# Kernel optimization log

Measured on AMD Instinct MI355X. Metric: run time of the kernel, lower is better.

## Reference

```python
import jax, jax.numpy as jnp
import numpy as np

DIM = 1024
N_HEADS = 16
HEAD_DIM = DIM // N_HEADS  # 64
B, T = 2, 2048


def setup_inputs() -> dict:
    key = jax.random.key(0)
    k1, k2, k3, k4, k5 = jax.random.split(key, 5)
    x = jax.random.normal(k1, (B, T, DIM), dtype=jnp.float32)
    cos = jax.random.uniform(k2, (1, 1, T, HEAD_DIM // 2), dtype=jnp.float32)
    sin = jax.random.uniform(k3, (1, 1, T, HEAD_DIM // 2), dtype=jnp.float32)
    # torch Linear weights: y = x @ W.T ; qkv: [3*dim, dim], out_proj: [dim, dim]
    w_qkv = jax.random.normal(k4, (3 * DIM, DIM), dtype=jnp.float32) * 0.02
    w_out = jax.random.normal(k5, (DIM, DIM), dtype=jnp.float32) * 0.02
    return {"x": x, "cos": cos, "sin": sin, "w_qkv": w_qkv, "w_out": w_out}


def _rope(t, cos, sin):
    # t: [B, H, T, D]; cos/sin broadcast as [1,1,T,D/2]
    t1, t2 = jnp.split(t, 2, axis=-1)
    return jnp.concatenate([t1 * cos - t2 * sin, t1 * sin + t2 * cos], axis=-1)


def reference(x, cos, sin, w_qkv, w_out):
    Bb, Tt, C = x.shape
    qkv = x @ w_qkv.T                                    # [B, T, 3C]
    q, k, v = jnp.split(qkv, 3, axis=-1)
    def heads(t):
        return t.reshape(Bb, Tt, N_HEADS, HEAD_DIM).transpose(0, 2, 1, 3)
    q, k, v = heads(q), heads(k), heads(v)               # [B, H, T, D]
    q = _rope(q, cos, sin)
    k = _rope(k, cos, sin)
    scale = 1.0 / jnp.sqrt(jnp.float32(HEAD_DIM))
    scores = jnp.einsum("bhqd,bhkd->bhqk", q, k) * scale  # [B, H, T, T]
    causal = jnp.tril(jnp.ones((Tt, Tt), dtype=bool))
    scores = jnp.where(causal[None, None], scores, jnp.float32(-jnp.inf))
    attn = jax.nn.softmax(scores, axis=-1)
    out = jnp.einsum("bhqk,bhkd->bhqd", attn, v)          # [B, H, T, D]
    out = out.transpose(0, 2, 1, 3).reshape(Bb, Tt, C)
    return out @ w_out.T
```

## Files before the change

kernel.cpp:

```cpp
#include <hip/hip_runtime.h>

#define DIMC 1024
#define NH   16
#define HD   64
#define BSZ  2
#define TSZ  2048
#define MROWS (BSZ*TSZ)

typedef __attribute__((ext_vector_type(8))) short s16x8;
typedef __attribute__((ext_vector_type(4))) float f32x4;

__device__ __forceinline__ float b2f(unsigned short u) {
  return __uint_as_float(((unsigned)u) << 16);
}
__device__ __forceinline__ unsigned short f2b(float f) {
  unsigned x = __float_as_uint(f);
  unsigned r = x + 0x7fffu + ((x >> 16) & 1u);
  return (unsigned short)(r >> 16);
}
__device__ __forceinline__ unsigned pk2(float a, float b) {
  unsigned r;
  asm("v_cvt_pk_bf16_f32 %0, %1, %2" : "=v"(r) : "v"(a), "v"(b));
  return r;
}
__device__ __forceinline__ float ex2(float x) {
#if __has_builtin(__builtin_amdgcn_exp2f)
  return __builtin_amdgcn_exp2f(x);
#else
  float r; asm("v_exp_f32 %0, %1" : "=v"(r) : "v"(x)); return r;
#endif
}
__device__ __forceinline__ float ldsc(const void* __restrict__ p, int idx, int isf32) {
  return isf32 ? ((const float*)p)[idx] : b2f(((const unsigned short*)p)[idx]);
}

__device__ __forceinline__ void async_cp16(const unsigned short* g, unsigned short* l) {
  __builtin_amdgcn_global_load_lds(
      (const __attribute__((address_space(1))) unsigned int*)g,
      (__attribute__((address_space(3))) unsigned int*)l, 16, 0, 0);
}

__global__ void detect_dtype(const unsigned short* __restrict__ cosp, int* __restrict__ flag) {
  const int i = threadIdx.x;
  const unsigned long long m = __ballot(cosp[i] >= 0x4000u);
  if (i == 0) *flag = (m != 0ull) ? 1 : 0;
}

__global__ __launch_bounds__(256)
void cvt_all(const float* __restrict__ x, const float* __restrict__ wq,
             const float* __restrict__ wo,
             unsigned short* __restrict__ xb, unsigned short* __restrict__ wqb,
             unsigned short* __restrict__ wob, const int* __restrict__ flag) {
  if (*flag == 0) return;
  const unsigned id = blockIdx.x * 256 + threadIdx.x;
  const float* src; unsigned short* dst; unsigned off;
  if (id < 524288u) { src = x; dst = xb; off = id; }
  else if (id < 917504u) { src = wq; dst = wqb; off = id - 524288u; }
  else { src = wo; dst = wob; off = id - 917504u; }
  const float4 a = ((const float4*)src)[off * 2];
  const float4 b = ((const float4*)src)[off * 2 + 1];
  uint4 u;
  u.x = pk2(a.x, a.y); u.y = pk2(a.z, a.w);
  u.z = pk2(b.x, b.y); u.w = pk2(b.z, b.w);
  ((uint4*)dst)[off] = u;
}

__global__ __launch_bounds__(512, 4)
void gemm_qkv128(const void* __restrict__ Aorig, const unsigned short* __restrict__ Aconv,
                 const void* __restrict__ Worig, const unsigned short* __restrict__ Wconv,
                 const void* __restrict__ cosp, const void* __restrict__ sinp,
                 unsigned short* __restrict__ qout,
                 unsigned short* __restrict__ kout,
                 unsigned short* __restrict__ vout,
                 const int* __restrict__ dflag) {
  const int f32flag = *dflag;
  const unsigned short* A = f32flag ? Aconv : (const unsigned short*)Aorig;
  const unsigned short* W = f32flag ? Wconv : (const unsigned short*)Worig;

  const int tid = threadIdx.x;
  const int m0 = blockIdx.y * 128;
  const int n0 = blockIdx.x * 128;

  __shared__ __align__(16) unsigned short s_ab[2 * 16384];

  const int lane = tid & 63;
  const int wave = tid >> 6;
  const int wm = (wave & 3) * 32;
  const int wn = (wave >> 2) * 64;
  const int m16 = lane & 15;
  const int quad = lane >> 4;

  const int srow = lane >> 3;
  const int schunk = (lane & 7) ^ srow;

  const unsigned short* ga = A + (size_t)(m0 + wave * 8 + srow) * DIMC + schunk * 8;
  const unsigned short* gb = W + (size_t)(n0 + wave * 8 + srow) * DIMC + schunk * 8;

  f32x4 acc[2][4];
#pragma unroll
  for (int i = 0; i < 2; ++i)
#pragma unroll
    for (int j = 0; j < 4; ++j) acc[i][j] = (f32x4){0.f, 0.f, 0.f, 0.f};

  auto stage = [&](int b, int kt) {
    unsigned short* sa = s_ab + b * 16384;
#pragma unroll
    for (int u = 0; u < 2; ++u) {
      async_cp16(ga + (size_t)(u * 64) * DIMC + kt, &sa[(u * 64 + wave * 8) * 64]);
      async_cp16(gb + (size_t)(u * 64) * DIMC + kt, &sa[8192 + (u * 64 + wave * 8) * 64]);
    }
  };

  stage(0, 0);
  __syncthreads();

  for (int t = 0; t < 16; ++t) {
    const int cur = t & 1;
    if (t < 15) stage(cur ^ 1, (t + 1) * 64);
    const unsigned short* sa = s_ab + cur * 16384;
    const unsigned short* sb = sa + 8192;
    __builtin_amdgcn_s_setprio(1);
#pragma unroll
    for (int kk = 0; kk < 64; kk += 32) {
      const int cx = ((kk >> 3) + quad) ^ (m16 & 7);
      s16x8 af[2], bf[4];
#pragma unroll
      for (int i = 0; i < 2; ++i)
        af[i] = *(const s16x8*)&sa[(wm + i * 16 + m16) * 64 + cx * 8];
#pragma unroll
      for (int j = 0; j < 4; ++j)
        bf[j] = *(const s16x8*)&sb[(wn + j * 16 + m16) * 64 + cx * 8];
#pragma unroll
      for (int i = 0; i < 2; ++i)
#pragma unroll
        for (int j = 0; j < 4; ++j)
          acc[i][j] = __builtin_amdgcn_mfma_f32_16x16x32_bf16(af[i], bf[j], acc[i][j], 0, 0, 0);
    }
    __builtin_amdgcn_s_setprio(0);
    __syncthreads();
  }

  const int sel = n0 >> 10;
  const int h = ((n0 & 1023) >> 6) + (wave >> 2);
  unsigned short* dst = (sel == 0) ? qout : ((sel == 1) ? kout : vout);
  const float qsc = (sel == 0) ? 0.18033688f : 1.0f;
  unsigned short* tile = s_ab + wave * 2048;
  if (sel < 2) {
#pragma unroll
    for (int i = 0; i < 2; ++i)
#pragma unroll
      for (int r = 0; r < 4; ++r) {
        const int row_l = i * 16 + quad * 4 + r;
        const int t = (m0 + wm + row_l) & 2047;
#pragma unroll
        for (int jg = 0; jg < 2; ++jg) {
          const int d = jg * 16 + m16;
          const float c = ldsc(cosp, t * 32 + d, f32flag);
          const float sn = ldsc(sinp, t * 32 + d, f32flag);
          const float v1 = acc[i][jg][r];
          const float v2 = acc[i][jg + 2][r];
          tile[row_l * 64 + d]      = f2b((v1 * c - v2 * sn) * qsc);
          tile[row_l * 64 + d + 32] = f2b((v1 * sn + v2 * c) * qsc);
        }
      }
  } else {
#pragma unroll
    for (int i = 0; i < 2; ++i)
#pragma unroll
      for (int r = 0; r < 4; ++r) {
        const int row_l = i * 16 + quad * 4 + r;
#pragma unroll
        for (int j = 0; j < 4; ++j)
          tile[row_l * 64 + j * 16 + m16] = f2b(acc[i][j][r]);
      }
  }
#pragma unroll
  for (int s = 0; s < 4; ++s) {
    const int row_l = s * 8 + (lane >> 3);
    const int seg = lane & 7;
    const int mrow_ = m0 + wm + row_l;
    const int bb = mrow_ >> 11;
    const int t = mrow_ & 2047;
    unsigned short* drow = dst + (((size_t)(bb * NH + h)) * TSZ + t) * HD;
    *(uint4*)(drow + seg * 8) = *(const uint4*)&tile[row_l * 64 + seg * 8];
  }
}

__global__ __launch_bounds__(256)
void gemm_out(const void* __restrict__ Aorig, const unsigned short* __restrict__ Aconv,
              const void* __restrict__ Worig, const unsigned short* __restrict__ Wconv,
              void* __restrict__ C, const int* __restrict__ dflag, int Nsz) {
  const int f32flag = *dflag;
  const unsigned short* A = f32flag ? Aconv : (const unsigned short*)Aorig;
  const unsigned short* W = f32flag ? Wconv : (const unsigned short*)Worig;

  const int tid = threadIdx.x;
  const int m0 = blockIdx.y * 128;
  const int n0 = blockIdx.x * 64;

  __shared__ __align__(16) unsigned short s_ab[2 * 12288];

  const int lane = tid & 63;
  const int wave = tid >> 6;
  const int wm = wave * 32;
  const int m16 = lane & 15;
  const int quad = lane >> 4;

  const int srow = lane >> 3;
  const int schunk = (lane & 7) ^ srow;

  const unsigned short* ga = A + (size_t)(m0 + wave * 8 + srow) * DIMC + schunk * 8;
  const unsigned short* gb = W + (size_t)(n0 + wave * 8 + srow) * DIMC + schunk * 8;

  f32x4 acc[2][4];
#pragma unroll
  for (int i = 0; i < 2; ++i)
#pragma unroll
    for (int j = 0; j < 4; ++j) acc[i][j] = (f32x4){0.f, 0.f, 0.f, 0.f};

  auto stage = [&](int b, int kt) {
    unsigned short* sa = s_ab + b * 12288;
#pragma unroll
    for (int u = 0; u < 4; ++u)
      async_cp16(ga + (size_t)(u * 32) * DIMC + kt, &sa[(u * 32 + wave * 8) * 64]);
#pragma unroll
    for (int u = 0; u < 2; ++u)
      async_cp16(gb + (size_t)(u * 32) * DIMC + kt, &sa[8192 + (u * 32 + wave * 8) * 64]);
  };

  stage(0, 0);
  __syncthreads();

  for (int t = 0; t < 16; ++t) {
    const int cur = t & 1;
    if (t < 15) stage(cur ^ 1, (t + 1) * 64);
    const unsigned short* sa = s_ab + cur * 12288;
    const unsigned short* sb = sa + 8192;
    __builtin_amdgcn_s_setprio(1);
#pragma unroll
    for (int kk = 0; kk < 64; kk += 32) {
      const int cx = ((kk >> 3) + quad) ^ (m16 & 7);
      s16x8 af[2], bf[4];
#pragma unroll
      for (int i = 0; i < 2; ++i)
        af[i] = *(const s16x8*)&sa[(wm + i * 16 + m16) * 64 + cx * 8];
#pragma unroll
      for (int j = 0; j < 4; ++j)
        bf[j] = *(const s16x8*)&sb[(j * 16 + m16) * 64 + cx * 8];
#pragma unroll
      for (int i = 0; i < 2; ++i)
#pragma unroll
        for (int j = 0; j < 4; ++j)
          acc[i][j] = __builtin_amdgcn_mfma_f32_16x16x32_bf16(af[i], bf[j], acc[i][j], 0, 0, 0);
    }
    __builtin_amdgcn_s_setprio(0);
    __syncthreads();
  }

  if (f32flag) {
    float* ftile = (float*)s_ab + wave * (32 * 68);
#pragma unroll
    for (int i = 0; i < 2; ++i)
#pragma unroll
      for (int j = 0; j < 4; ++j)
#pragma unroll
        for (int r = 0; r < 4; ++r)
          ftile[(i * 16 + quad * 4 + r) * 68 + j * 16 + m16] = acc[i][j][r];
    float* Cf = (float*)C;
#pragma unroll
    for (int i = 0; i < 2; ++i)
#pragma unroll
      for (int s = 0; s < 4; ++s) {
        const int row_l = i * 16 + s * 4 + (lane >> 4);
        const float4 vv = *(const float4*)&ftile[row_l * 68 + (lane & 15) * 4];
        *(float4*)&Cf[(size_t)(m0 + wm + row_l) * Nsz + n0 + (lane & 15) * 4] = vv;
      }
  } else {
    unsigned short* Ch = (unsigned short*)C;
#pragma unroll
    for (int i = 0; i < 2; ++i)
#pragma unroll
      for (int j = 0; j < 4; ++j)
#pragma unroll
        for (int r = 0; r < 4; ++r) {
          const int mrow_ = m0 + wm + i * 16 + quad * 4 + r;
          const int col = n0 + j * 16 + m16;
          Ch[(size_t)mrow_ * Nsz + col] = f2b(acc[i][j][r]);
        }
  }
}

__global__ __launch_bounds__(512, 4)
void attn_fwd_mfma(const unsigned short* __restrict__ qg,
                   const unsigned short* __restrict__ kg,
                   const unsigned short* __restrict__ vg,
                   unsigned short* __restrict__ outg) {
  const int tid = threadIdx.x;
  const int lane = tid & 63;
  const int w = tid >> 6;
  const int m16 = lane & 15;
  const int quad = lane >> 4;
  const int sw = m16 & 7;
  const int l = (int)blockIdx.x;
  const int g = (l & 255) >> 5;
  const int p = (l < 256) ? g : (15 - g);
  const int nc = (33 - p) >> 1;
  const int bh = l & 31;
  const int b = bh >> 4, h = bh & 15;
  const size_t base = (size_t)bh * TSZ * HD;
  const int sub = (w < 4) ? p : (31 - p);
  const int qs = sub * 64 + (w & 3) * 16;

  __shared__ __align__(16) unsigned short s_k[128 * 64];
  __shared__ __align__(16) unsigned short s_v[64 * 128];
  __shared__ __align__(16) unsigned short s_p[128 * 128];

  const unsigned short* qgh = qg + base;
  const unsigned short* kgh = kg + base;
  const unsigned short* vgh = vg + base;

  const unsigned short* qrow = qgh + (size_t)(qs + m16) * HD;
  const s16x8 bq0 = *(const s16x8*)(qrow + quad * 8);
  const s16x8 bq1 = *(const s16x8*)(qrow + 32 + quad * 8);

  f32x4 oacc[4];
#pragma unroll
  for (int dt = 0; dt < 4; ++dt) oacc[dt] = (f32x4){0.f, 0.f, 0.f, 0.f};
  float m_ = -1e30f, l_ = 0.f;

  const int krow = tid >> 3, kseg = tid & 7;
  const int vkey = tid & 63, vseg = tid >> 6;
  const int kcol = (kseg ^ (krow & 7)) * 8;
  const int vc0 = vkey >> 3, vo0 = vkey & 7;

  {
    const uint4 a0 = *(const uint4*)(kgh + (size_t)krow * HD + kseg * 8);
    const uint4 a1 = *(const uint4*)(kgh + (size_t)(64 + krow) * HD + kseg * 8);
    const uint4 b0 = *(const uint4*)(vgh + (size_t)vkey * HD + vseg * 8);
    const uint4 b1 = *(const uint4*)(vgh + (size_t)(64 + vkey) * HD + vseg * 8);
    *(uint4*)&s_k[krow * 64 + kcol] = a0;
    *(uint4*)&s_k[(64 + krow) * 64 + kcol] = a1;
    const unsigned short* v0 = (const unsigned short*)&b0;
    const unsigned short* v1 = (const unsigned short*)&b1;
#pragma unroll
    for (int jj = 0; jj < 8; ++jj) {
      const int dr = (vseg * 8 + jj) * 128;
      s_v[dr + (vc0 ^ jj) * 8 + vo0] = v0[jj];
      s_v[dr + ((8 + vc0) ^ jj) * 8 + vo0] = v1[jj];
    }
  }

  for (int kc = 0; kc < nc; ++kc) {
    __syncthreads();
    uint4 a0, a1, b0, b1;
    const int pf = (kc + 1 < nc);
    if (pf) {
      const size_t ko = (size_t)(kc + 1) * 128;
      a0 = *(const uint4*)(kgh + (ko + krow) * HD + kseg * 8);
      a1 = *(const uint4*)(kgh + (ko + 64 + krow) * HD + kseg * 8);
      b0 = *(const uint4*)(vgh + (ko + vkey) * HD + vseg * 8);
      b1 = *(const uint4*)(vgh + (ko + 64 + vkey) * HD + vseg * 8);
    }

    if (kc * 128 <= qs + 15) {
      f32x4 sacc[8];
#pragma unroll
      for (int jt = 0; jt < 8; ++jt) sacc[jt] = (f32x4){0.f, 0.f, 0.f, 0.f};
      __builtin_amdgcn_s_setprio(1);
#pragma unroll
      for (int jt = 0; jt < 8; ++jt) {
        const int krb = (jt * 16 + m16) * 64;
        const s16x8 ak0 = *(const s16x8*)&s_k[krb + (quad ^ sw) * 8];
        sacc[jt] = __builtin_amdgcn_mfma_f32_16x16x32_bf16(ak0, bq0, sacc[jt], 0, 0, 0);
        const s16x8 ak1 = *(const s16x8*)&s_k[krb + ((4 + quad) ^ sw) * 8];
        sacc[jt] = __builtin_amdgcn_mfma_f32_16x16x32_bf16(ak1, bq1, sacc[jt], 0, 0, 0);
      }
      __builtin_amdgcn_s_setprio(0);

      if (kc * 128 + 127 > qs) {
#pragma unroll
        for (int jt = 0; jt < 8; ++jt)
#pragma unroll
          for (int r = 0; r < 4; ++r)
            if (kc * 128 + jt * 16 + quad * 4 + r > qs + m16) sacc[jt][r] = -1e30f;
      }

      float mx = sacc[0][0];
#pragma unroll
      for (int jt = 0; jt < 8; ++jt)
#pragma unroll
        for (int r = 0; r < 4; ++r) mx = fmaxf(mx, sacc[jt][r]);
      mx = fmaxf(mx, __shfl_xor(mx, 16, 64));
      mx = fmaxf(mx, __shfl_xor(mx, 32, 64));
      if (!__all(mx <= m_ + 8.0f)) {
        const float mn = fmaxf(m_, mx);
        const float alpha = ex2(m_ - mn);
        m_ = mn;
        l_ *= alpha;
#pragma unroll
        for (int dt = 0; dt < 4; ++dt)
#pragma unroll
          for (int r = 0; r < 4; ++r) oacc[dt][r] *= alpha;
      }
      float rs = 0.f;
#pragma unroll
      for (int jt = 0; jt < 8; ++jt)
#pragma unroll
        for (int r = 0; r < 4; ++r) {
          const float pv_ = ex2(sacc[jt][r] - m_);
          sacc[jt][r] = pv_;
          rs += pv_;
        }
      rs += __shfl_xor(rs, 16, 64);
      rs += __shfl_xor(rs, 32, 64);
      l_ += rs;

      const int prb = (w * 16 + m16) * 128;
#pragma unroll
      for (int jt = 0; jt < 8; ++jt) {
        uint2 pw;
        pw.x = pk2(sacc[jt][0], sacc[jt][1]);
        pw.y = pk2(sacc[jt][2], sacc[jt][3]);
        *(uint2*)&s_p[prb + ((jt * 2 + (quad >> 1)) ^ sw) * 8 + (quad & 1) * 4] = pw;
      }

      __builtin_amdgcn_s_setprio(1);
#pragma unroll
      for (int kk = 0; kk < 128; kk += 32) {
        const int cx = (((kk >> 3) + quad) ^ sw) * 8;
        const s16x8 bp = *(const s16x8*)&s_p[prb + cx];
#pragma unroll
        for (int dt = 0; dt < 4; ++dt) {
          const s16x8 av = *(const s16x8*)&s_v[(dt * 16 + m16) * 128 + cx];
          oacc[dt] = __builtin_amdgcn_mfma_f32_16x16x32_bf16(av, bp, oacc[dt], 0, 0, 0);
        }
      }
      __builtin_amdgcn_s_setprio(0);
    }

    __syncthreads();
    if (pf) {
      *(uint4*)&s_k[krow * 64 + kcol] = a0;
      *(uint4*)&s_k[(64 + krow) * 64 + kcol] = a1;
      const unsigned short* v0 = (const unsigned short*)&b0;
      const unsigned short* v1 = (const unsigned short*)&b1;
#pragma unroll
      for (int jj = 0; jj < 8; ++jj) {
        const int dr = (vseg * 8 + jj) * 128;
        s_v[dr + (vc0 ^ jj) * 8 + vo0] = v0[jj];
        s_v[dr + ((8 + vc0) ^ jj) * 8 + vo0] = v1[jj];
      }
    }
  }

  const float linv = 1.0f / l_;
  {
    const int prb = (w * 16 + m16) * 128;
#pragma unroll
    for (int dt = 0; dt < 4; ++dt) {
      uint2 ow;
      ow.x = pk2(oacc[dt][0] * linv, oacc[dt][1] * linv);
      ow.y = pk2(oacc[dt][2] * linv, oacc[dt][3] * linv);
      *(uint2*)&s_p[prb + ((dt * 2 + (quad >> 1)) ^ sw) * 8 + (quad & 1) * 4] = ow;
    }
  }
  {
    const int qq = lane >> 2, dseg = lane & 3;
    const int swq = qq & 7;
    const int qrb = (w * 16 + qq) * 128;
    const uint4 o0 = *(const uint4*)&s_p[qrb + ((dseg * 2) ^ swq) * 8];
    const uint4 o1 = *(const uint4*)&s_p[qrb + ((dseg * 2 + 1) ^ swq) * 8];
    unsigned short* orow =
        outg + ((size_t)b * TSZ + qs + qq) * DIMC + h * 64 + dseg * 16;
    *(uint4*)orow = o0;
    *(uint4*)(orow + 8) = o1;
  }
}

extern "C" void kernel_launch(void* const* d_in, const int* in_sizes, int n_in,
                              void* d_out, int out_size, void* d_ws, size_t ws_size,
                              hipStream_t stream) {
  (void)in_sizes; (void)n_in; (void)out_size; (void)ws_size;
  const void* x    = d_in[0];
  const void* cosp = d_in[1];
  const void* sinp = d_in[2];
  const void* wqkv = d_in[3];
  const void* wout = d_in[4];

  int* dflag = (int*)d_ws;
  const size_t per = (size_t)BSZ * NH * TSZ * HD;
  unsigned short* q = (unsigned short*)((char*)d_ws + 256);
  unsigned short* k = q + per;
  unsigned short* v = k + per;
  unsigned short* attnb = v + per;
  unsigned short* xb   = attnb + (size_t)MROWS * DIMC;
  unsigned short* wqb  = xb + (size_t)MROWS * DIMC;
  unsigned short* wob  = wqb + (size_t)3 * DIMC * DIMC;

  detect_dtype<<<1, 64, 0, stream>>>((const unsigned short*)cosp, dflag);
  cvt_all<<<dim3(4096), dim3(256), 0, stream>>>(
      (const float*)x, (const float*)wqkv, (const float*)wout, xb, wqb, wob, dflag);
  gemm_qkv128<<<dim3(3 * DIMC / 128, MROWS / 128), dim3(512), 0, stream>>>(
      x, xb, wqkv, wqb, cosp, sinp, q, k, v, dflag);
  attn_fwd_mfma<<<dim3(512), dim3(512), 0, stream>>>(q, k, v, attnb);
  gemm_out<<<dim3(DIMC / 64, MROWS / 128), dim3(256), 0, stream>>>(
      attnb, attnb, wout, wob, d_out, dflag, DIMC);
}
```

Baseline: 175.7 us.

## Have each attention wave process two 16-row query tiles with 256-thread blocks

The attention kernel now runs 4 waves per block instead of 8, and each wave handles 32 query rows as two 16-row fragments. Each K and V fragment read from shared memory then feeds two MFMAs, which halves LDS reads per MFMA. Each thread also loads twice as much K/V per chunk. In exchange the kernel needs more registers per wave, and the causal-skip condition is coarser, so a wave may compute some fully masked tiles.

```diff
diff --git a/kernel.cpp b/kernel.cpp
--- a/kernel.cpp
+++ b/kernel.cpp
@@ -290,7 +290,7 @@
   }
 }
 
-__global__ __launch_bounds__(512, 4)
+__global__ __launch_bounds__(256, 2)
 void attn_fwd_mfma(const unsigned short* __restrict__ qg,
                    const unsigned short* __restrict__ kg,
                    const unsigned short* __restrict__ vg,
@@ -308,8 +308,8 @@
   const int bh = l & 31;
   const int b = bh >> 4, h = bh & 15;
   const size_t base = (size_t)bh * TSZ * HD;
-  const int sub = (w < 4) ? p : (31 - p);
-  const int qs = sub * 64 + (w & 3) * 16;
+  const int sub = (w < 2) ? p : (31 - p);
+  const int qs = sub * 64 + (w & 1) * 32;
 
   __shared__ __align__(16) unsigned short s_k[128 * 64];
   __shared__ __align__(16) unsigned short s_v[64 * 128];
@@ -319,120 +319,151 @@
   const unsigned short* kgh = kg + base;
   const unsigned short* vgh = vg + base;
 
-  const unsigned short* qrow = qgh + (size_t)(qs + m16) * HD;
-  const s16x8 bq0 = *(const s16x8*)(qrow + quad * 8);
-  const s16x8 bq1 = *(const s16x8*)(qrow + 32 + quad * 8);
-
-  f32x4 oacc[4];
-#pragma unroll
-  for (int dt = 0; dt < 4; ++dt) oacc[dt] = (f32x4){0.f, 0.f, 0.f, 0.f};
-  float m_ = -1e30f, l_ = 0.f;
+  s16x8 bq[2][2];
+#pragma unroll
+  for (int f = 0; f < 2; ++f) {
+    const unsigned short* qrow = qgh + (size_t)(qs + f * 16 + m16) * HD;
+    bq[f][0] = *(const s16x8*)(qrow + quad * 8);
+    bq[f][1] = *(const s16x8*)(qrow + 32 + quad * 8);
+  }
+
+  f32x4 oacc[2][4];
+#pragma unroll
+  for (int f = 0; f < 2; ++f)
+#pragma unroll
+    for (int dt = 0; dt < 4; ++dt) oacc[f][dt] = (f32x4){0.f, 0.f, 0.f, 0.f};
+  float m_[2] = {-1e30f, -1e30f}, l_[2] = {0.f, 0.f};
 
   const int krow = tid >> 3, kseg = tid & 7;
+  const int kcol = (kseg ^ (krow & 7)) * 8;
   const int vkey = tid & 63, vseg = tid >> 6;
-  const int kcol = (kseg ^ (krow & 7)) * 8;
   const int vc0 = vkey >> 3, vo0 = vkey & 7;
 
   {
-    const uint4 a0 = *(const uint4*)(kgh + (size_t)krow * HD + kseg * 8);
-    const uint4 a1 = *(const uint4*)(kgh + (size_t)(64 + krow) * HD + kseg * 8);
-    const uint4 b0 = *(const uint4*)(vgh + (size_t)vkey * HD + vseg * 8);
-    const uint4 b1 = *(const uint4*)(vgh + (size_t)(64 + vkey) * HD + vseg * 8);
-    *(uint4*)&s_k[krow * 64 + kcol] = a0;
-    *(uint4*)&s_k[(64 + krow) * 64 + kcol] = a1;
-    const unsigned short* v0 = (const unsigned short*)&b0;
-    const unsigned short* v1 = (const unsigned short*)&b1;
+    uint4 ka[4], vb[4];
+#pragma unroll
+    for (int u = 0; u < 4; ++u)
+      ka[u] = *(const uint4*)(kgh + (size_t)(krow + u * 32) * HD + kseg * 8);
+    vb[0] = *(const uint4*)(vgh + (size_t)vkey * HD + vseg * 8);
+    vb[1] = *(const uint4*)(vgh + (size_t)(64 + vkey) * HD + vseg * 8);
+    vb[2] = *(const uint4*)(vgh + (size_t)vkey * HD + (vseg + 4) * 8);
+    vb[3] = *(const uint4*)(vgh + (size_t)(64 + vkey) * HD + (vseg + 4) * 8);
+#pragma unroll
+    for (int u = 0; u < 4; ++u)
+      *(uint4*)&s_k[(krow + u * 32) * 64 + kcol] = ka[u];
 #pragma unroll
     for (int jj = 0; jj < 8; ++jj) {
-      const int dr = (vseg * 8 + jj) * 128;
-      s_v[dr + (vc0 ^ jj) * 8 + vo0] = v0[jj];
-      s_v[dr + ((8 + vc0) ^ jj) * 8 + vo0] = v1[jj];
+      const unsigned short* v0 = (const unsigned short*)&vb[0];
+      const unsigned short* v1 = (const unsigned short*)&vb[1];
+      const unsigned short* v2 = (const unsigned short*)&vb[2];
+      const unsigned short* v3 = (const unsigned short*)&vb[3];
+      const int dr0 = (vseg * 8 + jj) * 128;
+      const int dr1 = ((vseg + 4) * 8 + jj) * 128;
+      s_v[dr0 + (vc0 ^ jj) * 8 + vo0] = v0[jj];
+      s_v[dr0 + ((8 + vc0) ^ jj) * 8 + vo0] = v1[jj];
+      s_v[dr1 + (vc0 ^ jj) * 8 + vo0] = v2[jj];
+      s_v[dr1 + ((8 + vc0) ^ jj) * 8 + vo0] = v3[jj];
     }
   }
 
   for (int kc = 0; kc < nc; ++kc) {
     __syncthreads();
-    uint4 a0, a1, b0, b1;
+    uint4 ka[4], vb[4];
     const int pf = (kc + 1 < nc);
     if (pf) {
       const size_t ko = (size_t)(kc + 1) * 128;
-      a0 = *(const uint4*)(kgh + (ko + krow) * HD + kseg * 8);
-      a1 = *(const uint4*)(kgh + (ko + 64 + krow) * HD + kseg * 8);
-      b0 = *(const uint4*)(vgh + (ko + vkey) * HD + vseg * 8);
-      b1 = *(const uint4*)(vgh + (ko + 64 + vkey) * HD + vseg * 8);
-    }
-
-    if (kc * 128 <= qs + 15) {
-      f32x4 sacc[8];
-#pragma unroll
-      for (int jt = 0; jt < 8; ++jt) sacc[jt] = (f32x4){0.f, 0.f, 0.f, 0.f};
+#pragma unroll
+      for (int u = 0; u < 4; ++u)
+        ka[u] = *(const uint4*)(kgh + (ko + krow + u * 32) * HD + kseg * 8);
+      vb[0] = *(const uint4*)(vgh + (ko + vkey) * HD + vseg * 8);
+      vb[1] = *(const uint4*)(vgh + (ko + 64 + vkey) * HD + vseg * 8);
+      vb[2] = *(const uint4*)(vgh + (ko + vkey) * HD + (vseg + 4) * 8);
+      vb[3] = *(const uint4*)(vgh + (ko + 64 + vkey) * HD + (vseg + 4) * 8);
+    }
+
+    if (kc * 128 <= qs + 15 + 16) {
+      f32x4 sacc[2][8];
+#pragma unroll
+      for (int f = 0; f < 2; ++f)
+#pragma unroll
+        for (int jt = 0; jt < 8; ++jt) sacc[f][jt] = (f32x4){0.f, 0.f, 0.f, 0.f};
       __builtin_amdgcn_s_setprio(1);
 #pragma unroll
       for (int jt = 0; jt < 8; ++jt) {
         const int krb = (jt * 16 + m16) * 64;
         const s16x8 ak0 = *(const s16x8*)&s_k[krb + (quad ^ sw) * 8];
-        sacc[jt] = __builtin_amdgcn_mfma_f32_16x16x32_bf16(ak0, bq0, sacc[jt], 0, 0, 0);
+        sacc[0][jt] = __builtin_amdgcn_mfma_f32_16x16x32_bf16(ak0, bq[0][0], sacc[0][jt], 0, 0, 0);
+        sacc[1][jt] = __builtin_amdgcn_mfma_f32_16x16x32_bf16(ak0, bq[1][0], sacc[1][jt], 0, 0, 0);
         const s16x8 ak1 = *(const s16x8*)&s_k[krb + ((4 + quad) ^ sw) * 8];
-        sacc[jt] = __builtin_amdgcn_mfma_f32_16x16x32_bf16(ak1, bq1, sacc[jt], 0, 0, 0);
+        sacc[0][jt] = __builtin_amdgcn_mfma_f32_16x16x32_bf16(ak1, bq[0][1], sacc[0][jt], 0, 0, 0);
+        sacc[1][jt] = __builtin_amdgcn_mfma_f32_16x16x32_bf16(ak1, bq[1][1], sacc[1][jt], 0, 0, 0);
       }
       __builtin_amdgcn_s_setprio(0);
 
-      if (kc * 128 + 127 > qs) {
+      const int diag = (kc * 128 + 127 > qs);
+#pragma unroll
+      for (int f = 0; f < 2; ++f) {
+        const int qglob = qs + f * 16 + m16;
+        if (diag) {
+#pragma unroll
+          for (int jt = 0; jt < 8; ++jt)
+#pragma unroll
+            for (int r = 0; r < 4; ++r)
+              if (kc * 128 + jt * 16 + quad * 4 + r > qglob) sacc[f][jt][r] = -1e30f;
+        }
+        float mx = sacc[f][0][0];
 #pragma unroll
         for (int jt = 0; jt < 8; ++jt)
 #pragma unroll
-          for (int r = 0; r < 4; ++r)
-            if (kc * 128 + jt * 16 + quad * 4 + r > qs + m16) sacc[jt][r] = -1e30f;
-      }
-
-      float mx = sacc[0][0];
-#pragma unroll
-      for (int jt = 0; jt < 8; ++jt)
-#pragma unroll
-        for (int r = 0; r < 4; ++r) mx = fmaxf(mx, sacc[jt][r]);
-      mx = fmaxf(mx, __shfl_xor(mx, 16, 64));
-      mx = fmaxf(mx, __shfl_xor(mx, 32, 64));
-      if (!__all(mx <= m_ + 8.0f)) {
-        const float mn = fmaxf(m_, mx);
-        const float alpha = ex2(m_ - mn);
-        m_ = mn;
-        l_ *= alpha;
-#pragma unroll
-        for (int dt = 0; dt < 4; ++dt)
-#pragma unroll
-          for (int r = 0; r < 4; ++r) oacc[dt][r] *= alpha;
-      }
-      float rs = 0.f;
-#pragma unroll
-      for (int jt = 0; jt < 8; ++jt)
-#pragma unroll
-        for (int r = 0; r < 4; ++r) {
-          const float pv_ = ex2(sacc[jt][r] - m_);
-          sacc[jt][r] = pv_;
-          rs += pv_;
+          for (int r = 0; r < 4; ++r) mx = fmaxf(mx, sacc[f][jt][r]);
+        mx = fmaxf(mx, __shfl_xor(mx, 16, 64));
+        mx = fmaxf(mx, __shfl_xor(mx, 32, 64));
+        if (!__all(mx <= m_[f] + 8.0f)) {
+          const float mn = fmaxf(m_[f], mx);
+          const float alpha = ex2(m_[f] - mn);
+          m_[f] = mn;
+          l_[f] *= alpha;
+#pragma unroll
+          for (int dt = 0; dt < 4; ++dt)
+#pragma unroll
+            for (int r = 0; r < 4; ++r) oacc[f][dt][r] *= alpha;
         }
-      rs += __shfl_xor(rs, 16, 64);
-      rs += __shfl_xor(rs, 32, 64);
-      l_ += rs;
-
-      const int prb = (w * 16 + m16) * 128;
-#pragma unroll
-      for (int jt = 0; jt < 8; ++jt) {
-        uint2 pw;
-        pw.x = pk2(sacc[jt][0], sacc[jt][1]);
-        pw.y = pk2(sacc[jt][2], sacc[jt][3]);
-        *(uint2*)&s_p[prb + ((jt * 2 + (quad >> 1)) ^ sw) * 8 + (quad & 1) * 4] = pw;
-      }
-
+        float rs = 0.f;
+#pragma unroll
+        for (int jt = 0; jt < 8; ++jt)
+#pragma unroll
+          for (int r = 0; r < 4; ++r) {
+            const float pv_ = ex2(sacc[f][jt][r] - m_[f]);
+            sacc[f][jt][r] = pv_;
+            rs += pv_;
+          }
+        rs += __shfl_xor(rs, 16, 64);
+        rs += __shfl_xor(rs, 32, 64);
+        l_[f] += rs;
+
+        const int prb = (w * 32 + f * 16 + m16) * 128;
+#pragma unroll
+        for (int jt = 0; jt < 8; ++jt) {
+          uint2 pw;
+          pw.x = pk2(sacc[f][jt][0], sacc[f][jt][1]);
+          pw.y = pk2(sacc[f][jt][2], sacc[f][jt][3]);
+          *(uint2*)&s_p[prb + ((jt * 2 + (quad >> 1)) ^ sw) * 8 + (quad & 1) * 4] = pw;
+        }
+      }
+
+      const int prb0 = (w * 32 + m16) * 128;
+      const int prb1 = (w * 32 + 16 + m16) * 128;
       __builtin_amdgcn_s_setprio(1);
 #pragma unroll
       for (int kk = 0; kk < 128; kk += 32) {
         const int cx = (((kk >> 3) + quad) ^ sw) * 8;
-        const s16x8 bp = *(const s16x8*)&s_p[prb + cx];
+        const s16x8 bp0 = *(const s16x8*)&s_p[prb0 + cx];
+        const s16x8 bp1 = *(const s16x8*)&s_p[prb1 + cx];
 #pragma unroll
         for (int dt = 0; dt < 4; ++dt) {
           const s16x8 av = *(const s16x8*)&s_v[(dt * 16 + m16) * 128 + cx];
-          oacc[dt] = __builtin_amdgcn_mfma_f32_16x16x32_bf16(av, bp, oacc[dt], 0, 0, 0);
+          oacc[0][dt] = __builtin_amdgcn_mfma_f32_16x16x32_bf16(av, bp0, oacc[0][dt], 0, 0, 0);
+          oacc[1][dt] = __builtin_amdgcn_mfma_f32_16x16x32_bf16(av, bp1, oacc[1][dt], 0, 0, 0);
         }
       }
       __builtin_amdgcn_s_setprio(0);
@@ -440,38 +471,46 @@
 
     __syncthreads();
     if (pf) {
-      *(uint4*)&s_k[krow * 64 + kcol] = a0;
-      *(uint4*)&s_k[(64 + krow) * 64 + kcol] = a1;
-      const unsigned short* v0 = (const unsigned short*)&b0;
-      const unsigned short* v1 = (const unsigned short*)&b1;
+#pragma unroll
+      for (int u = 0; u < 4; ++u)
+        *(uint4*)&s_k[(krow + u * 32) * 64 + kcol] = ka[u];
 #pragma unroll
       for (int jj = 0; jj < 8; ++jj) {
-        const int dr = (vseg * 8 + jj) * 128;
-        s_v[dr + (vc0 ^ jj) * 8 + vo0] = v0[jj];
-        s_v[dr + ((8 + vc0) ^ jj) * 8 + vo0] = v1[jj];
-      }
-    }
-  }
-
-  const float linv = 1.0f / l_;
-  {
-    const int prb = (w * 16 + m16) * 128;
+        const unsigned short* v0 = (const unsigned short*)&vb[0];
+        const unsigned short* v1 = (const unsigned short*)&vb[1];
+        const unsigned short* v2 = (const unsigned short*)&vb[2];
+        const unsigned short* v3 = (const unsigned short*)&vb[3];
+        const int dr0 = (vseg * 8 + jj) * 128;
+        const int dr1 = ((vseg + 4) * 8 + jj) * 128;
+        s_v[dr0 + (vc0 ^ jj) * 8 + vo0] = v0[jj];
+        s_v[dr0 + ((8 + vc0) ^ jj) * 8 + vo0] = v1[jj];
+        s_v[dr1 + (vc0 ^ jj) * 8 + vo0] = v2[jj];
+        s_v[dr1 + ((8 + vc0) ^ jj) * 8 + vo0] = v3[jj];
+      }
+    }
+  }
+
+#pragma unroll
+  for (int f = 0; f < 2; ++f) {
+    const float linv = 1.0f / l_[f];
+    const int prb = (w * 32 + f * 16 + m16) * 128;
 #pragma unroll
     for (int dt = 0; dt < 4; ++dt) {
       uint2 ow;
-      ow.x = pk2(oacc[dt][0] * linv, oacc[dt][1] * linv);
-      ow.y = pk2(oacc[dt][2] * linv, oacc[dt][3] * linv);
+      ow.x = pk2(oacc[f][dt][0] * linv, oacc[f][dt][1] * linv);
+      ow.y = pk2(oacc[f][dt][2] * linv, oacc[f][dt][3] * linv);
       *(uint2*)&s_p[prb + ((dt * 2 + (quad >> 1)) ^ sw) * 8 + (quad & 1) * 4] = ow;
     }
   }
-  {
+#pragma unroll
+  for (int f = 0; f < 2; ++f) {
     const int qq = lane >> 2, dseg = lane & 3;
     const int swq = qq & 7;
-    const int qrb = (w * 16 + qq) * 128;
+    const int qrb = (w * 32 + f * 16 + qq) * 128;
     const uint4 o0 = *(const uint4*)&s_p[qrb + ((dseg * 2) ^ swq) * 8];
     const uint4 o1 = *(const uint4*)&s_p[qrb + ((dseg * 2 + 1) ^ swq) * 8];
     unsigned short* orow =
-        outg + ((size_t)b * TSZ + qs + qq) * DIMC + h * 64 + dseg * 16;
+        outg + ((size_t)b * TSZ + qs + f * 16 + qq) * DIMC + h * 64 + dseg * 16;
     *(uint4*)orow = o0;
     *(uint4*)(orow + 8) = o1;
   }
@@ -502,7 +541,7 @@
       (const float*)x, (const float*)wqkv, (const float*)wout, xb, wqb, wob, dflag);
   gemm_qkv128<<<dim3(3 * DIMC / 128, MROWS / 128), dim3(512), 0, stream>>>(
       x, xb, wqkv, wqb, cosp, sinp, q, k, v, dflag);
-  attn_fwd_mfma<<<dim3(512), dim3(512), 0, stream>>>(q, k, v, attnb);
+  attn_fwd_mfma<<<dim3(512), dim3(256), 0, stream>>>(q, k, v, attnb);
   gemm_out<<<dim3(DIMC / 64, MROWS / 128), dim3(256), 0, stream>>>(
       attnb, attnb, wout, wob, d_out, dflag, DIMC);
 }
```

Measured after the change: 213.3 us. 21.4% more time.
